# Performance work log

Hardware: AMD Instinct MI355X
Metric: run time of the kernel (lower is better)

Reference implementation:

```python
import jax, jax.numpy as jnp
import numpy as np
from jax import lax

B, T, F, H, L = 64, 2048, 128, 128, 2


def _lstm_layer(x, Wih, Whh, bih, bhh, h0, c0):
    """Single LSTM layer, torch gate order (i,f,g,o). x: [B,T,in] -> y: [B,T,H], hT, cT."""
    b = bih + bhh

    def step(carry, xt):
        h, c = carry
        gates = xt @ Wih.T + h @ Whh.T + b  # [B,4H]
        i, f, g, o = jnp.split(gates, 4, axis=-1)
        i = jax.nn.sigmoid(i)
        f = jax.nn.sigmoid(f)
        g = jnp.tanh(g)
        o = jax.nn.sigmoid(o)
        c = f * c + i * g
        h = o * jnp.tanh(c)
        return (h, c), h

    xs = jnp.swapaxes(x, 0, 1)  # [T,B,in]
    (hT, cT), ys = lax.scan(step, (h0, c0), xs)
    return jnp.swapaxes(ys, 0, 1), hT, cT


def setup_inputs() -> dict:
    key = jax.random.key(0)
    ks = jax.random.split(key, 20)
    s = 1.0 / np.sqrt(H)
    u = lambda k, shape: jax.random.uniform(k, shape, jnp.float32, -s, s)
    inp = {"x": jax.random.normal(ks[0], (B, T, F), jnp.float32)}
    i = 1
    for pre, in0 in (("enc", F), ("dec", H)):
        for l in range(L):
            d_in = in0 if l == 0 else H
            inp[f"{pre}_Wih{l}"] = u(ks[i], (4 * H, d_in)); i += 1
            inp[f"{pre}_Whh{l}"] = u(ks[i], (4 * H, H)); i += 1
            inp[f"{pre}_bih{l}"] = u(ks[i], (4 * H,)); i += 1
            inp[f"{pre}_bhh{l}"] = u(ks[i], (4 * H,)); i += 1
    inp["out_W"] = u(ks[i], (F, H)); i += 1
    inp["out_b"] = u(ks[i], (F,))
    return inp


def reference(x,
              enc_Wih0, enc_Whh0, enc_bih0, enc_bhh0,
              enc_Wih1, enc_Whh1, enc_bih1, enc_bhh1,
              dec_Wih0, dec_Whh0, dec_bih0, dec_bhh0,
              dec_Wih1, dec_Whh1, dec_bih1, dec_bhh1,
              out_W, out_b):
    z = jnp.zeros((x.shape[0], H), x.dtype)
    # encoder: 2 stacked layers, zero initial state
    y0, h0, c0 = _lstm_layer(x, enc_Wih0, enc_Whh0, enc_bih0, enc_bhh0, z, z)
    y1, h1, c1 = _lstm_layer(y0, enc_Wih1, enc_Whh1, enc_bih1, enc_bhh1, z, z)
    # decoder: zeros input, initial state = encoder final (h,c) per layer
    dec_in = jnp.zeros_like(x)  # valid since n_features == hidden_dim
    d0, _, _ = _lstm_layer(dec_in, dec_Wih0, dec_Whh0, dec_bih0, dec_bhh0, h0, c0)
    d1, _, _ = _lstm_layer(d0, dec_Wih1, dec_Whh1, dec_bih1, dec_bhh1, h1, c1)
    return d1 @ out_W.T + out_b
```

## Files before the change

kernel.cpp:

```cpp
#include <hip/hip_runtime.h>
#include <cstdint>
#include <cstddef>

typedef float    float4v __attribute__((ext_vector_type(4)));
typedef _Float16 f16x4   __attribute__((ext_vector_type(4)));
typedef _Float16 f16x8   __attribute__((ext_vector_type(8)));
typedef unsigned long long u64;
struct u64p { u64 a, b; };

#define DI __device__ __forceinline__

static const int Bsz = 64, Tlen = 2048, Hd = 128;
static const int HSTR = 144;
static const int RING = 256;
static const int YSTR = 136;

DI float sigf_fast(float x) {
    float e = __builtin_amdgcn_exp2f(-1.442695041f * x);
    return __builtin_amdgcn_rcpf(1.f + e);
}
DI float tanhf_fast(float x) {
    float e = __builtin_amdgcn_exp2f(-2.885390082f * x);
    return 2.f * __builtin_amdgcn_rcpf(1.f + e) - 1.f;
}

DI void lds_barrier() {
    asm volatile("s_waitcnt lgkmcnt(0)\n\ts_barrier" ::: "memory");
}

DI void pin(f16x8& v) {
    float4v t = __builtin_bit_cast(float4v, v);
    asm volatile("" : "+v"(t));
    v = __builtin_bit_cast(f16x8, t);
}

DI f16x8 cvt8(const float* p) {
    float4v u = *(const float4v*)p;
    float4v w = *(const float4v*)(p + 4);
    f16x8 o;
    o[0] = (_Float16)u[0]; o[1] = (_Float16)u[1]; o[2] = (_Float16)u[2]; o[3] = (_Float16)u[3];
    o[4] = (_Float16)w[0]; o[5] = (_Float16)w[1]; o[6] = (_Float16)w[2]; o[7] = (_Float16)w[3];
    return o;
}

DI u64 pack4(float4v a) {
    f16x4 h;
    h[0] = (_Float16)a[0]; h[1] = (_Float16)a[1];
    h[2] = (_Float16)a[2]; h[3] = (_Float16)a[3];
    return __builtin_bit_cast(u64, h);
}

DI u64 ald64(const void* pp) {
    return __hip_atomic_load((const u64*)pp, __ATOMIC_RELAXED, __HIP_MEMORY_SCOPE_AGENT);
}
DI void ast64(void* pp, u64 v) {
    __hip_atomic_store((u64*)pp, v, __ATOMIC_RELAXED, __HIP_MEMORY_SCOPE_AGENT);
}
DI void ast16(void* pp, unsigned short v) {
    __hip_atomic_store((unsigned short*)pp, v, __ATOMIC_RELAXED, __HIP_MEMORY_SCOPE_AGENT);
}
DI unsigned int aldu32(const unsigned int* pp) {
    return __hip_atomic_load(pp, __ATOMIC_RELAXED, __HIP_MEMORY_SCOPE_AGENT);
}
DI void astu32(unsigned int* pp, unsigned int v) {
    __hip_atomic_store(pp, v, __ATOMIC_RELAXED, __HIP_MEMORY_SCOPE_AGENT);
}

__global__ __launch_bounds__(512, 1) void lstm_mega(
    const float* __restrict__ eU0, const float* __restrict__ eb0i, const float* __restrict__ eb0h,
    const float* __restrict__ dU0, const float* __restrict__ db0i, const float* __restrict__ db0h,
    const float* __restrict__ eU1, const float* __restrict__ eb1i, const float* __restrict__ eb1h,
    const float* __restrict__ dU1, const float* __restrict__ db1i, const float* __restrict__ db1h,
    const float* __restrict__ eW1, const float* __restrict__ dW1,
    const float* __restrict__ eW0, const float* __restrict__ xin,
    const float* __restrict__ oW,  const float* __restrict__ ob,
    float* __restrict__ outp,
    _Float16* __restrict__ PB,
    _Float16* __restrict__ X2,
    _Float16* __restrict__ X1,
    _Float16* __restrict__ Y1,
    unsigned int* __restrict__ prog,  unsigned int* __restrict__ prog2,
    unsigned int* __restrict__ prog3, unsigned int* __restrict__ prog4,
    unsigned int* __restrict__ prog5, int T)
{
    const int tid  = threadIdx.x;
    const int lane = tid & 63, w = tid >> 6;
    const int col  = lane & 15, quad = lane >> 4;
    const int b    = col & 3, s = col >> 2;
    const int role = blockIdx.x >> 4;
    const int p    = blockIdx.x & 15;
    const int bglob = p * 4 + b;
    const int j    = w * 16 + s * 4 + quad;
    const int NG   = T >> 3;
    const int NG2  = NG * 2;
    const unsigned int T2 = (unsigned int)(2 * T);

    __shared__ alignas(16) _Float16 Hl[2 * 4 * HSTR];
    __shared__ alignas(16) _Float16 Ylh[32 * YSTR];

    unsigned int* pr  = prog  + p * 16;
    unsigned int* pr2 = prog2 + p * 16;
    unsigned int* pr3 = prog3 + p * 16;
    unsigned int* pr4 = prog4 + p * 16;
    unsigned int* pr5 = prog5 + p * 16;

    if (role == 0) {
        f16x8 af[4][4];
        float bq[4];
#pragma unroll
        for (int mt = 0; mt < 4; mt++) {
            int urow = (col & 3) * 128 + (w * 16 + mt * 4 + (col >> 2));
            const float* ur = eU0 + (size_t)urow * 128;
#pragma unroll
            for (int kc = 0; kc < 4; kc++) { af[mt][kc] = cvt8(ur + kc * 32 + quad * 8); pin(af[mt][kc]); }
        }
#pragma unroll
        for (int q = 0; q < 4; q++) bq[q] = eb0i[q * 128 + j] + eb0h[q * 128 + j];

        float c = 0.f, hv = 0.f;
        Hl[b * HSTR + j] = (_Float16)0.f;
        __syncthreads();

        const _Float16* x1b = X1 + (size_t)bglob * RING * 512 + 4 * j;
        unsigned short* pbp = (unsigned short*)PB + (size_t)bglob * RING * 128 + j;

        if (tid == 511) {
            unsigned int need = 16u; if (need > (unsigned int)T) need = (unsigned int)T;
            unsigned int psn = aldu32(pr3);
            while (psn < need) { __builtin_amdgcn_s_sleep(8); psn = aldu32(pr3); }
        }
        __syncthreads();
        f16x4 xp = __builtin_bit_cast(f16x4, ald64(x1b));

        int cur = 0;
        unsigned int pf3 = 0, ps3 = 0;
        for (int g = 0; g < NG2; g++) {
            if (g == NG) {
#pragma unroll
                for (int mt = 0; mt < 4; mt++) {
                    int urow = (col & 3) * 128 + (w * 16 + mt * 4 + (col >> 2));
                    const float* ur = dU0 + (size_t)urow * 128;
#pragma unroll
                    for (int kc = 0; kc < 4; kc++) { af[mt][kc] = cvt8(ur + kc * 32 + quad * 8); pin(af[mt][kc]); }
                }
#pragma unroll
                for (int q = 0; q < 4; q++) bq[q] = db0i[q * 128 + j] + db0h[q * 128 + j];
            }
            if (g < NG) {
                if (tid == 511 && g + 1 < NG) pf3 = aldu32(pr3);
#pragma unroll
                for (int k = 0; k < 8; k++) {
                    const int t = g * 8 + k;
                    f16x4 xpn = __builtin_bit_cast(f16x4,
                        ald64(x1b + (size_t)((t + 1) & (RING - 1)) * 512));

                    const _Float16* Hc = Hl + cur * (4 * HSTR);
                    f16x8 bf[4];
#pragma unroll
                    for (int kc = 0; kc < 4; kc++)
                        bf[kc] = *(const f16x8*)(Hc + b * HSTR + kc * 32 + quad * 8);

                    float4v acc[4] = {};
#pragma unroll
                    for (int kc = 0; kc < 4; kc++)
#pragma unroll
                        for (int mt = 0; mt < 4; mt++)
                            acc[mt] = __builtin_amdgcn_mfma_f32_16x16x32_f16(af[mt][kc], bf[kc], acc[mt], 0, 0, 0);

                    float4v t0 = (s & 1) ? acc[1] : acc[0];
                    float4v t1 = (s & 1) ? acc[3] : acc[2];
                    float4v gg = (s & 2) ? t1 : t0;

                    float g0 = gg[0] + bq[0] + (float)xp[0], g1 = gg[1] + bq[1] + (float)xp[1];
                    float g2 = gg[2] + bq[2] + (float)xp[2], g3 = gg[3] + bq[3] + (float)xp[3];
                    float iv = sigf_fast(g0), fv = sigf_fast(g1);
                    float gv = tanhf_fast(g2), ov = sigf_fast(g3);
                    c  = fv * c + iv * gv;
                    hv = ov * tanhf_fast(c);

                    _Float16 hf = (_Float16)hv;
                    Hl[(cur ^ 1) * (4 * HSTR) + b * HSTR + j] = hf;
                    ast16(pbp + (size_t)(t & (RING - 1)) * 128,
                          __builtin_bit_cast(unsigned short, hf));

                    if (k == 7) {
                        asm volatile("s_waitcnt vmcnt(2)" ::: "memory");
                        if (tid == 0) astu32(pr, (unsigned int)(g * 8 + 7));
                        if (tid == 511 && g + 1 < NG) {
                            unsigned int need = (unsigned int)(8 * (g + 1) + 16);
                            if (need > (unsigned int)T) need = (unsigned int)T;
                            if (ps3 < pf3) ps3 = pf3;
                            while (ps3 < need) { __builtin_amdgcn_s_sleep(2); ps3 = aldu32(pr3); }
                        }
                    }
                    lds_barrier();
                    xp = xpn;
                    cur ^= 1;
                }
            } else {
#pragma unroll
                for (int k = 0; k < 8; k++) {
                    const int t = g * 8 + k;

                    const _Float16* Hc = Hl + cur * (4 * HSTR);
                    f16x8 bf[4];
#pragma unroll
                    for (int kc = 0; kc < 4; kc++)
                        bf[kc] = *(const f16x8*)(Hc + b * HSTR + kc * 32 + quad * 8);

                    float4v acc[4] = {};
#pragma unroll
                    for (int kc = 0; kc < 4; kc++)
#pragma unroll
                        for (int mt = 0; mt < 4; mt++)
                            acc[mt] = __builtin_amdgcn_mfma_f32_16x16x32_f16(af[mt][kc], bf[kc], acc[mt], 0, 0, 0);

                    float4v t0 = (s & 1) ? acc[1] : acc[0];
                    float4v t1 = (s & 1) ? acc[3] : acc[2];
                    float4v gg = (s & 2) ? t1 : t0;

                    float g0 = gg[0] + bq[0], g1 = gg[1] + bq[1];
                    float g2 = gg[2] + bq[2], g3 = gg[3] + bq[3];
                    float iv = sigf_fast(g0), fv = sigf_fast(g1);
                    float gv = tanhf_fast(g2), ov = sigf_fast(g3);
                    c  = fv * c + iv * gv;
                    hv = ov * tanhf_fast(c);

                    _Float16 hf = (_Float16)hv;
                    Hl[(cur ^ 1) * (4 * HSTR) + b * HSTR + j] = hf;
                    ast16(pbp + (size_t)(t & (RING - 1)) * 128,
                          __builtin_bit_cast(unsigned short, hf));

                    if (k == 7) {
                        asm volatile("s_waitcnt vmcnt(1)" ::: "memory");
                        if (tid == 0) astu32(pr, (unsigned int)(g * 8 + 7));
                    }
                    lds_barrier();
                    cur ^= 1;
                }
            }
        }
        asm volatile("s_waitcnt vmcnt(0)" ::: "memory");
        __syncthreads();
        if (tid == 0) astu32(pr, T2);
    } else if (role == 1) {
        f16x8 afH[4][4];
        float bq[4];
#pragma unroll
        for (int mt = 0; mt < 4; mt++) {
            int urow = (col & 3) * 128 + (w * 16 + mt * 4 + (col >> 2));
            const float* ur = eU1 + (size_t)urow * 128;
#pragma unroll
            for (int kc = 0; kc < 4; kc++) { afH[mt][kc] = cvt8(ur + kc * 32 + quad * 8); pin(afH[mt][kc]); }
        }
#pragma unroll
        for (int q = 0; q < 4; q++) bq[q] = eb1i[q * 128 + j] + eb1h[q * 128 + j];

        float c = 0.f, hv = 0.f;
        Hl[b * HSTR + j] = (_Float16)0.f;

        if (tid == 511) {
            unsigned int need = 9u; if (need > T2) need = T2;
            unsigned int psn = aldu32(pr2);
            while (psn < need) { __builtin_amdgcn_s_sleep(8); psn = aldu32(pr2); }
        }
        __syncthreads();

        const _Float16* x2b = X2 + (size_t)bglob * RING * 512 + 4 * j;
        unsigned short* y1p = (unsigned short*)Y1 + (size_t)bglob * RING * 128 + j;
        f16x4 xp = __builtin_bit_cast(f16x4, ald64(x2b));

        int cur = 0;
        unsigned int pf2 = 0, ps2 = 0, pf5 = 0, ps5 = 0;
        for (int g = 0; g < NG2; g++) {
            if (g == NG) {
#pragma unroll
                for (int mt = 0; mt < 4; mt++) {
                    int urow = (col & 3) * 128 + (w * 16 + mt * 4 + (col >> 2));
                    const float* ur = dU1 + (size_t)urow * 128;
#pragma unroll
                    for (int kc = 0; kc < 4; kc++) { afH[mt][kc] = cvt8(ur + kc * 32 + quad * 8); pin(afH[mt][kc]); }
                }
#pragma unroll
                for (int q = 0; q < 4; q++) bq[q] = db1i[q * 128 + j] + db1h[q * 128 + j];
            }
            if (tid == 511) {
                if (g + 1 < NG2) pf2 = aldu32(pr2);
                if (g + 1 >= NG + 32 && g + 1 < NG2) pf5 = aldu32(pr5);
            }
            if (g < NG) {
#pragma unroll
                for (int k = 0; k < 8; k++) {
                    const int t = g * 8 + k;
                    f16x4 xpn = __builtin_bit_cast(f16x4,
                        ald64(x2b + (size_t)((t + 1) & (RING - 1)) * 512));

                    const _Float16* Hc = Hl + cur * (4 * HSTR);
                    f16x8 bf[4];
#pragma unroll
                    for (int kc = 0; kc < 4; kc++)
                        bf[kc] = *(const f16x8*)(Hc + b * HSTR + kc * 32 + quad * 8);

                    float4v acc[4] = {};
#pragma unroll
                    for (int kc = 0; kc < 4; kc++)
#pragma unroll
                        for (int mt = 0; mt < 4; mt++)
                            acc[mt] = __builtin_amdgcn_mfma_f32_16x16x32_f16(afH[mt][kc], bf[kc], acc[mt], 0, 0, 0);

                    float4v t0 = (s & 1) ? acc[1] : acc[0];
                    float4v t1 = (s & 1) ? acc[3] : acc[2];
                    float4v gg = (s & 2) ? t1 : t0;

                    float g0 = gg[0] + bq[0] + (float)xp[0], g1 = gg[1] + bq[1] + (float)xp[1];
                    float g2 = gg[2] + bq[2] + (float)xp[2], g3 = gg[3] + bq[3] + (float)xp[3];
                    float iv = sigf_fast(g0), fv = sigf_fast(g1);
                    float gv = tanhf_fast(g2), ov = sigf_fast(g3);
                    c  = fv * c + iv * gv;
                    hv = ov * tanhf_fast(c);

                    Hl[(cur ^ 1) * (4 * HSTR) + b * HSTR + j] = (_Float16)hv;

                    if (k == 7) {
                        if (tid == 511 && g + 1 < NG2) {
                            unsigned int need = (unsigned int)(8 * (g + 1) + 9);
                            if (need > T2) need = T2;
                            if (ps2 < pf2) ps2 = pf2;
                            while (ps2 < need) { __builtin_amdgcn_s_sleep(2); ps2 = aldu32(pr2); }
                        }
                    }
                    lds_barrier();
                    xp = xpn;
                    cur ^= 1;
                }
            } else {
#pragma unroll
                for (int k = 0; k < 8; k++) {
                    const int t = g * 8 + k;
                    f16x4 xpn = __builtin_bit_cast(f16x4,
                        ald64(x2b + (size_t)((t + 1) & (RING - 1)) * 512));

                    const _Float16* Hc = Hl + cur * (4 * HSTR);
                    f16x8 bf[4];
#pragma unroll
                    for (int kc = 0; kc < 4; kc++)
                        bf[kc] = *(const f16x8*)(Hc + b * HSTR + kc * 32 + quad * 8);

                    float4v acc[4] = {};
#pragma unroll
                    for (int kc = 0; kc < 4; kc++)
#pragma unroll
                        for (int mt = 0; mt < 4; mt++)
                            acc[mt] = __builtin_amdgcn_mfma_f32_16x16x32_f16(afH[mt][kc], bf[kc], acc[mt], 0, 0, 0);

                    float4v t0 = (s & 1) ? acc[1] : acc[0];
                    float4v t1 = (s & 1) ? acc[3] : acc[2];
                    float4v gg = (s & 2) ? t1 : t0;

                    float g0 = gg[0] + bq[0] + (float)xp[0], g1 = gg[1] + bq[1] + (float)xp[1];
                    float g2 = gg[2] + bq[2] + (float)xp[2], g3 = gg[3] + bq[3] + (float)xp[3];
                    float iv = sigf_fast(g0), fv = sigf_fast(g1);
                    float gv = tanhf_fast(g2), ov = sigf_fast(g3);
                    c  = fv * c + iv * gv;
                    hv = ov * tanhf_fast(c);

                    _Float16 hf = (_Float16)hv;
                    Hl[(cur ^ 1) * (4 * HSTR) + b * HSTR + j] = hf;
                    ast16(y1p + (size_t)(t & (RING - 1)) * 128,
                          __builtin_bit_cast(unsigned short, hf));

                    if (k == 7) {
                        asm volatile("s_waitcnt vmcnt(2)" ::: "memory");
                        if (tid == 0) astu32(pr4, (unsigned int)(g * 8 + 7));
                        if (tid == 511 && g + 1 < NG2) {
                            unsigned int need = (unsigned int)(8 * (g + 1) + 9);
                            if (need > T2) need = T2;
                            if (ps2 < pf2) ps2 = pf2;
                            while (ps2 < need) { __builtin_amdgcn_s_sleep(2); ps2 = aldu32(pr2); }
                            if (g + 1 >= NG + 32) {
                                unsigned int need5 = (unsigned int)(8 * (g + 1 - 32) + 8);
                                if (ps5 < pf5) ps5 = pf5;
                                while (ps5 < need5) { __builtin_amdgcn_s_sleep(2); ps5 = aldu32(pr5); }
                            }
                        }
                    }
                    lds_barrier();
                    xp = xpn;
                    cur ^= 1;
                }
            }
        }
        asm volatile("s_waitcnt vmcnt(0)" ::: "memory");
        __syncthreads();
        if (tid == 0) astu32(pr4, T2);
    } else if (role == 2) {
        f16x8 bw[4][4];
#pragma unroll
        for (int nt = 0; nt < 4; nt++) {
            int n = (w * 4 + nt) * 16 + col;
            int wrow = (n & 3) * 128 + (n >> 2);
            const float* Wr = eW1 + (size_t)wrow * 128;
#pragma unroll
            for (int kc = 0; kc < 4; kc++) { bw[nt][kc] = cvt8(Wr + kc * 32 + quad * 8); pin(bw[nt][kc]); }
        }

        const int lrow = tid >> 4, lchunk = tid & 15;
        const int lb = lrow & 3, ltr = lrow >> 2;

        for (int g = 0; g < NG2; g++) {
            if (g == NG) {
#pragma unroll
                for (int nt = 0; nt < 4; nt++) {
                    int n = (w * 4 + nt) * 16 + col;
                    int wrow = (n & 3) * 128 + (n >> 2);
                    const float* Wr = dW1 + (size_t)wrow * 128;
#pragma unroll
                    for (int kc = 0; kc < 4; kc++) { bw[nt][kc] = cvt8(Wr + kc * 32 + quad * 8); pin(bw[nt][kc]); }
                }
            }
            if (tid == 0) {
                unsigned int need = (unsigned int)(g * 8 + 8);
                unsigned int psn = aldu32(pr);
                while (psn < need) { __builtin_amdgcn_s_sleep(4); psn = aldu32(pr); }
            }
            __syncthreads();
            {
                int slot = (g * 8 + ltr) & (RING - 1);
                const char* srcp = (const char*)(PB + ((size_t)(p * 4 + lb) * RING + slot) * 128 + lchunk * 8);
                u64 a0 = ald64(srcp);
                u64 a1 = ald64(srcp + 8);
                char* dst = (char*)&Ylh[lrow * YSTR + lchunk * 8];
                *(u64*)dst = a0;
                *(u64*)(dst + 8) = a1;
            }
            lds_barrier();

            float4v acc[2][4] = {};
#pragma unroll
            for (int kc = 0; kc < 4; kc++) {
                f16x8 y0 = *(const f16x8*)&Ylh[col * YSTR + kc * 32 + quad * 8];
                f16x8 y1t = *(const f16x8*)&Ylh[(16 + col) * YSTR + kc * 32 + quad * 8];
#pragma unroll
                for (int nt = 0; nt < 4; nt++) {
                    acc[0][nt] = __builtin_amdgcn_mfma_f32_16x16x32_f16(bw[nt][kc], y0,  acc[0][nt], 0, 0, 0);
                    acc[1][nt] = __builtin_amdgcn_mfma_f32_16x16x32_f16(bw[nt][kc], y1t, acc[1][nt], 0, 0, 0);
                }
            }
            {
                const int bb = col & 3;
#pragma unroll
                for (int mt = 0; mt < 2; mt++) {
                    int trow = mt * 4 + (col >> 2);
                    int slot = (g * 8 + trow) & (RING - 1);
                    _Float16* dst = X2 + ((size_t)(p * 4 + bb) * RING + slot) * 512 + (w * 4) * 16 + quad * 4;
#pragma unroll
                    for (int nt = 0; nt < 4; nt++)
                        ast64(dst + nt * 16, pack4(acc[mt][nt]));
                }
            }
            asm volatile("s_waitcnt vmcnt(0)" ::: "memory");
            __syncthreads();
            if (tid == 0) astu32(pr2, (unsigned int)(g * 8 + 8));
        }
    } else if (role == 3) {
        f16x8 bw[4][4];
#pragma unroll
        for (int nt = 0; nt < 4; nt++) {
            int n = (w * 4 + nt) * 16 + col;
            int wrow = (n & 3) * 128 + (n >> 2);
            const float* Wr = eW0 + (size_t)wrow * 128;
#pragma unroll
            for (int kc = 0; kc < 4; kc++) { bw[nt][kc] = cvt8(Wr + kc * 32 + quad * 8); pin(bw[nt][kc]); }
        }

        const int lrow = tid >> 4, lchunk = tid & 15;
        const int lb = lrow & 3, ltr = lrow >> 2;
        const float* xsrc = xin + (size_t)(p * 4 + lb) * T * 128 + lchunk * 8;

        for (int g = 0; g < NG; g++) {
            if (g >= 32 && tid == 0) {
                unsigned int need = (unsigned int)(8 * (g - 32));
                unsigned int psn = aldu32(pr);
                while (psn < need) { __builtin_amdgcn_s_sleep(4); psn = aldu32(pr); }
            }
            __syncthreads();
            {
                f16x8 xv = cvt8(xsrc + (size_t)(g * 8 + ltr) * 128);
                u64p w2 = __builtin_bit_cast(u64p, xv);
                char* dst = (char*)&Ylh[lrow * YSTR + lchunk * 8];
                *(u64*)dst = w2.a;
                *(u64*)(dst + 8) = w2.b;
            }
            lds_barrier();

            float4v acc[2][4] = {};
#pragma unroll
            for (int kc = 0; kc < 4; kc++) {
                f16x8 y0 = *(const f16x8*)&Ylh[col * YSTR + kc * 32 + quad * 8];
                f16x8 y1t = *(const f16x8*)&Ylh[(16 + col) * YSTR + kc * 32 + quad * 8];
#pragma unroll
                for (int nt = 0; nt < 4; nt++) {
                    acc[0][nt] = __builtin_amdgcn_mfma_f32_16x16x32_f16(bw[nt][kc], y0,  acc[0][nt], 0, 0, 0);
                    acc[1][nt] = __builtin_amdgcn_mfma_f32_16x16x32_f16(bw[nt][kc], y1t, acc[1][nt], 0, 0, 0);
                }
            }
            {
                const int bb = col & 3;
#pragma unroll
                for (int mt = 0; mt < 2; mt++) {
                    int trow = mt * 4 + (col >> 2);
                    int slot = (g * 8 + trow) & (RING - 1);
                    _Float16* dst = X1 + ((size_t)(p * 4 + bb) * RING + slot) * 512 + (w * 4) * 16 + quad * 4;
#pragma unroll
                    for (int nt = 0; nt < 4; nt++)
                        ast64(dst + nt * 16, pack4(acc[mt][nt]));
                }
            }
            asm volatile("s_waitcnt vmcnt(0)" ::: "memory");
            __syncthreads();
            if (tid == 0) astu32(pr3, (unsigned int)(g * 8 + 8));
        }
    } else {
        f16x8 bo[4];
#pragma unroll
        for (int kc = 0; kc < 4; kc++) { bo[kc] = cvt8(oW + (size_t)(w * 16 + col) * 128 + kc * 32 + quad * 8); pin(bo[kc]); }
        float4v bv4 = *(const float4v*)(ob + w * 16 + quad * 4);

        const int lrow = tid >> 4, lchunk = tid & 15;
        const int lb = lrow & 3, ltr = lrow >> 2;

        for (int gg = 0; gg < NG; gg++) {
            const int g = NG + gg;
            if (tid == 0) {
                unsigned int need = (unsigned int)(g * 8 + 8);
                unsigned int psn = aldu32(pr4);
                while (psn < need) { __builtin_amdgcn_s_sleep(4); psn = aldu32(pr4); }
            }
            __syncthreads();
            {
                int slot = (g * 8 + ltr) & (RING - 1);
                const char* srcp = (const char*)(Y1 + ((size_t)(p * 4 + lb) * RING + slot) * 128 + lchunk * 8);
                u64 a0 = ald64(srcp);
                u64 a1 = ald64(srcp + 8);
                char* dst = (char*)&Ylh[lrow * YSTR + lchunk * 8];
                *(u64*)dst = a0;
                *(u64*)(dst + 8) = a1;
            }
            lds_barrier();
            if (tid == 0) astu32(pr5, (unsigned int)(g * 8 + 8));

            float4v acc[2] = {};
#pragma unroll
            for (int kc = 0; kc < 4; kc++) {
                f16x8 y0 = *(const f16x8*)&Ylh[col * YSTR + kc * 32 + quad * 8];
                f16x8 y1t = *(const f16x8*)&Ylh[(16 + col) * YSTR + kc * 32 + quad * 8];
                acc[0] = __builtin_amdgcn_mfma_f32_16x16x32_f16(bo[kc], y0,  acc[0], 0, 0, 0);
                acc[1] = __builtin_amdgcn_mfma_f32_16x16x32_f16(bo[kc], y1t, acc[1], 0, 0, 0);
            }
            {
                const int bb = col & 3;
#pragma unroll
                for (int mt = 0; mt < 2; mt++) {
                    int trow = mt * 4 + (col >> 2);
                    float4v v = acc[mt];
                    v[0] += bv4[0]; v[1] += bv4[1]; v[2] += bv4[2]; v[3] += bv4[3];
                    *(float4v*)(outp + ((size_t)(p * 4 + bb) * T + gg * 8 + trow) * 128 + w * 16 + quad * 4) = v;
                }
            }
        }
    }
}

extern "C" void kernel_launch(void* const* d_in, const int* in_sizes, int n_in,
                              void* d_out, int out_size, void* d_ws, size_t ws_size,
                              hipStream_t stream)
{
    const float* x    = (const float*)d_in[0];
    const float* eW0  = (const float*)d_in[1];
    const float* eU0  = (const float*)d_in[2];
    const float* eb0i = (const float*)d_in[3];
    const float* eb0h = (const float*)d_in[4];
    const float* eW1  = (const float*)d_in[5];
    const float* eU1  = (const float*)d_in[6];
    const float* eb1i = (const float*)d_in[7];
    const float* eb1h = (const float*)d_in[8];
    const float* dU0  = (const float*)d_in[10];
    const float* db0i = (const float*)d_in[11];
    const float* db0h = (const float*)d_in[12];
    const float* dW1  = (const float*)d_in[13];
    const float* dU1  = (const float*)d_in[14];
    const float* db1i = (const float*)d_in[15];
    const float* db1h = (const float*)d_in[16];
    const float* oW   = (const float*)d_in[17];
    const float* ob   = (const float*)d_in[18];

    char* ws = (char*)d_ws;
    _Float16* X1 = (_Float16*)(ws);
    _Float16* X2 = (_Float16*)(ws + (16u << 20));
    _Float16* PB = (_Float16*)(ws + (32u << 20));
    _Float16* Y1 = (_Float16*)(ws + (36u << 20));
    unsigned int* pg = (unsigned int*)(ws + (40u << 20));

    hipMemsetAsync((void*)pg, 0, 8192, stream);

    lstm_mega<<<dim3(80), dim3(512), 0, stream>>>(
        eU0, eb0i, eb0h, dU0, db0i, db0h,
        eU1, eb1i, eb1h, dU1, db1i, db1h,
        eW1, dW1, eW0, x, oW, ob, (float*)d_out,
        PB, X2, X1, Y1,
        pg, pg + 256, pg + 512, pg + 768, pg + 1024, Tlen);
}
```

Before: 2.400 ms.

## Halve block size to 256 threads, each thread computing two hidden units

```diff
diff --git a/kernel.cpp b/kernel.cpp
--- a/kernel.cpp
+++ b/kernel.cpp
@@ -66,7 +66,7 @@
     __hip_atomic_store(pp, v, __ATOMIC_RELAXED, __HIP_MEMORY_SCOPE_AGENT);
 }
 
-__global__ __launch_bounds__(512, 1) void lstm_mega(
+__global__ __launch_bounds__(256, 1) void lstm_mega(
     const float* __restrict__ eU0, const float* __restrict__ eb0i, const float* __restrict__ eb0h,
     const float* __restrict__ dU0, const float* __restrict__ db0i, const float* __restrict__ db0h,
     const float* __restrict__ eU1, const float* __restrict__ eb1i, const float* __restrict__ eb1h,
@@ -90,7 +90,8 @@
     const int role = blockIdx.x >> 4;
     const int p    = blockIdx.x & 15;
     const int bglob = p * 4 + b;
-    const int j    = w * 16 + s * 4 + quad;
+    const int jA   = w * 32 + s * 4 + quad;
+    const int jB   = jA + 16;
     const int NG   = T >> 3;
     const int NG2  = NG * 2;
     const unsigned int T2 = (unsigned int)(2 * T);
@@ -105,54 +106,65 @@
     unsigned int* pr5 = prog5 + p * 16;
 
     if (role == 0) {
-        f16x8 af[4][4];
-        float bq[4];
-#pragma unroll
-        for (int mt = 0; mt < 4; mt++) {
-            int urow = (col & 3) * 128 + (w * 16 + mt * 4 + (col >> 2));
+        f16x8 af[8][4];
+        float bqA[4], bqB[4];
+#pragma unroll
+        for (int mt = 0; mt < 8; mt++) {
+            int urow = (col & 3) * 128 + (w * 32 + mt * 4 + (col >> 2));
             const float* ur = eU0 + (size_t)urow * 128;
 #pragma unroll
             for (int kc = 0; kc < 4; kc++) { af[mt][kc] = cvt8(ur + kc * 32 + quad * 8); pin(af[mt][kc]); }
         }
 #pragma unroll
-        for (int q = 0; q < 4; q++) bq[q] = eb0i[q * 128 + j] + eb0h[q * 128 + j];
-
-        float c = 0.f, hv = 0.f;
-        Hl[b * HSTR + j] = (_Float16)0.f;
+        for (int q = 0; q < 4; q++) {
+            bqA[q] = eb0i[q * 128 + jA] + eb0h[q * 128 + jA];
+            bqB[q] = eb0i[q * 128 + jB] + eb0h[q * 128 + jB];
+        }
+
+        float cA = 0.f, hA = 0.f, cB = 0.f, hB = 0.f;
+        Hl[b * HSTR + jA] = (_Float16)0.f;
+        Hl[b * HSTR + jB] = (_Float16)0.f;
         __syncthreads();
 
-        const _Float16* x1b = X1 + (size_t)bglob * RING * 512 + 4 * j;
-        unsigned short* pbp = (unsigned short*)PB + (size_t)bglob * RING * 128 + j;
-
-        if (tid == 511) {
+        const _Float16* x1bA = X1 + (size_t)bglob * RING * 512 + 4 * jA;
+        const _Float16* x1bB = x1bA + 64;
+        unsigned short* pbpA = (unsigned short*)PB + (size_t)bglob * RING * 128 + jA;
+        unsigned short* pbpB = pbpA + 16;
+
+        if (tid == 255) {
             unsigned int need = 16u; if (need > (unsigned int)T) need = (unsigned int)T;
             unsigned int psn = aldu32(pr3);
             while (psn < need) { __builtin_amdgcn_s_sleep(8); psn = aldu32(pr3); }
         }
         __syncthreads();
-        f16x4 xp = __builtin_bit_cast(f16x4, ald64(x1b));
+        f16x4 xpA = __builtin_bit_cast(f16x4, ald64(x1bA));
+        f16x4 xpB = __builtin_bit_cast(f16x4, ald64(x1bB));
 
         int cur = 0;
         unsigned int pf3 = 0, ps3 = 0;
         for (int g = 0; g < NG2; g++) {
             if (g == NG) {
 #pragma unroll
-                for (int mt = 0; mt < 4; mt++) {
-                    int urow = (col & 3) * 128 + (w * 16 + mt * 4 + (col >> 2));
+                for (int mt = 0; mt < 8; mt++) {
+                    int urow = (col & 3) * 128 + (w * 32 + mt * 4 + (col >> 2));
                     const float* ur = dU0 + (size_t)urow * 128;
 #pragma unroll
                     for (int kc = 0; kc < 4; kc++) { af[mt][kc] = cvt8(ur + kc * 32 + quad * 8); pin(af[mt][kc]); }
                 }
 #pragma unroll
-                for (int q = 0; q < 4; q++) bq[q] = db0i[q * 128 + j] + db0h[q * 128 + j];
+                for (int q = 0; q < 4; q++) {
+                    bqA[q] = db0i[q * 128 + jA] + db0h[q * 128 + jA];
+                    bqB[q] = db0i[q * 128 + jB] + db0h[q * 128 + jB];
+                }
             }
             if (g < NG) {
-                if (tid == 511 && g + 1 < NG) pf3 = aldu32(pr3);
+                if (tid == 255 && g + 1 < NG) pf3 = aldu32(pr3);
 #pragma unroll
                 for (int k = 0; k < 8; k++) {
                     const int t = g * 8 + k;
-                    f16x4 xpn = __builtin_bit_cast(f16x4,
-                        ald64(x1b + (size_t)((t + 1) & (RING - 1)) * 512));
+                    const size_t nsl = (size_t)((t + 1) & (RING - 1)) * 512;
+                    f16x4 xpnA = __builtin_bit_cast(f16x4, ald64(x1bA + nsl));
+                    f16x4 xpnB = __builtin_bit_cast(f16x4, ald64(x1bB + nsl));
 
                     const _Float16* Hc = Hl + cur * (4 * HSTR);
                     f16x8 bf[4];
@@ -160,33 +172,46 @@
                     for (int kc = 0; kc < 4; kc++)
                         bf[kc] = *(const f16x8*)(Hc + b * HSTR + kc * 32 + quad * 8);
 
-                    float4v acc[4] = {};
+                    float4v acc[8] = {};
 #pragma unroll
                     for (int kc = 0; kc < 4; kc++)
 #pragma unroll
-                        for (int mt = 0; mt < 4; mt++)
+                        for (int mt = 0; mt < 8; mt++)
                             acc[mt] = __builtin_amdgcn_mfma_f32_16x16x32_f16(af[mt][kc], bf[kc], acc[mt], 0, 0, 0);
 
-                    float4v t0 = (s & 1) ? acc[1] : acc[0];
-                    float4v t1 = (s & 1) ? acc[3] : acc[2];
-                    float4v gg = (s & 2) ? t1 : t0;
-
-                    float g0 = gg[0] + bq[0] + (float)xp[0], g1 = gg[1] + bq[1] + (float)xp[1];
-                    float g2 = gg[2] + bq[2] + (float)xp[2], g3 = gg[3] + bq[3] + (float)xp[3];
-                    float iv = sigf_fast(g0), fv = sigf_fast(g1);
-                    float gv = tanhf_fast(g2), ov = sigf_fast(g3);
-                    c  = fv * c + iv * gv;
-                    hv = ov * tanhf_fast(c);
-
-                    _Float16 hf = (_Float16)hv;
-                    Hl[(cur ^ 1) * (4 * HSTR) + b * HSTR + j] = hf;
-                    ast16(pbp + (size_t)(t & (RING - 1)) * 128,
-                          __builtin_bit_cast(unsigned short, hf));
+                    float4v u0 = (s & 1) ? acc[1] : acc[0];
+                    float4v u1 = (s & 1) ? acc[3] : acc[2];
+                    float4v gA = (s & 2) ? u1 : u0;
+                    float4v u2 = (s & 1) ? acc[5] : acc[4];
+                    float4v u3 = (s & 1) ? acc[7] : acc[6];
+                    float4v gB = (s & 2) ? u3 : u2;
+
+                    float a0 = gA[0] + bqA[0] + (float)xpA[0], a1 = gA[1] + bqA[1] + (float)xpA[1];
+                    float a2 = gA[2] + bqA[2] + (float)xpA[2], a3 = gA[3] + bqA[3] + (float)xpA[3];
+                    float iA = sigf_fast(a0), fA = sigf_fast(a1);
+                    float gvA = tanhf_fast(a2), oA = sigf_fast(a3);
+                    cA = fA * cA + iA * gvA;
+                    hA = oA * tanhf_fast(cA);
+
+                    float b0 = gB[0] + bqB[0] + (float)xpB[0], b1 = gB[1] + bqB[1] + (float)xpB[1];
+                    float b2 = gB[2] + bqB[2] + (float)xpB[2], b3 = gB[3] + bqB[3] + (float)xpB[3];
+                    float iB = sigf_fast(b0), fB = sigf_fast(b1);
+                    float gvB = tanhf_fast(b2), oB = sigf_fast(b3);
+                    cB = fB * cB + iB * gvB;
+                    hB = oB * tanhf_fast(cB);
+
+                    _Float16 hfA = (_Float16)hA, hfB = (_Float16)hB;
+                    _Float16* Hn = Hl + (cur ^ 1) * (4 * HSTR) + b * HSTR;
+                    Hn[jA] = hfA;
+                    Hn[jB] = hfB;
+                    const size_t sl = (size_t)(t & (RING - 1)) * 128;
+                    ast16(pbpA + sl, __builtin_bit_cast(unsigned short, hfA));
+                    ast16(pbpB + sl, __builtin_bit_cast(unsigned short, hfB));
 
                     if (k == 7) {
-                        asm volatile("s_waitcnt vmcnt(2)" ::: "memory");
+                        asm volatile("s_waitcnt vmcnt(4)" ::: "memory");
                         if (tid == 0) astu32(pr, (unsigned int)(g * 8 + 7));
-                        if (tid == 511 && g + 1 < NG) {
+                        if (tid == 255 && g + 1 < NG) {
                             unsigned int need = (unsigned int)(8 * (g + 1) + 16);
                             if (need > (unsigned int)T) need = (unsigned int)T;
                             if (ps3 < pf3) ps3 = pf3;
@@ -194,7 +219,7 @@
                         }
                     }
                     lds_barrier();
-                    xp = xpn;
+                    xpA = xpnA; xpB = xpnB;
                     cur ^= 1;
                 }
             } else {
@@ -208,31 +233,44 @@
                     for (int kc = 0; kc < 4; kc++)
                         bf[kc] = *(const f16x8*)(Hc + b * HSTR + kc * 32 + quad * 8);
 
-                    float4v acc[4] = {};
+                    float4v acc[8] = {};
 #pragma unroll
                     for (int kc = 0; kc < 4; kc++)
 #pragma unroll
-                        for (int mt = 0; mt < 4; mt++)
+                        for (int mt = 0; mt < 8; mt++)
                             acc[mt] = __builtin_amdgcn_mfma_f32_16x16x32_f16(af[mt][kc], bf[kc], acc[mt], 0, 0, 0);
 
-                    float4v t0 = (s & 1) ? acc[1] : acc[0];
-                    float4v t1 = (s & 1) ? acc[3] : acc[2];
-                    float4v gg = (s & 2) ? t1 : t0;
-
-                    float g0 = gg[0] + bq[0], g1 = gg[1] + bq[1];
-                    float g2 = gg[2] + bq[2], g3 = gg[3] + bq[3];
-                    float iv = sigf_fast(g0), fv = sigf_fast(g1);
-                    float gv = tanhf_fast(g2), ov = sigf_fast(g3);
-                    c  = fv * c + iv * gv;
-                    hv = ov * tanhf_fast(c);
-
-                    _Float16 hf = (_Float16)hv;
-                    Hl[(cur ^ 1) * (4 * HSTR) + b * HSTR + j] = hf;
-                    ast16(pbp + (size_t)(t & (RING - 1)) * 128,
-                          __builtin_bit_cast(unsigned short, hf));
+                    float4v u0 = (s & 1) ? acc[1] : acc[0];
+                    float4v u1 = (s & 1) ? acc[3] : acc[2];
+                    float4v gA = (s & 2) ? u1 : u0;
+                    float4v u2 = (s & 1) ? acc[5] : acc[4];
+                    float4v u3 = (s & 1) ? acc[7] : acc[6];
+                    float4v gB = (s & 2) ? u3 : u2;
+
+                    float a0 = gA[0] + bqA[0], a1 = gA[1] + bqA[1];
+                    float a2 = gA[2] + bqA[2], a3 = gA[3] + bqA[3];
+                    float iA = sigf_fast(a0), fA = sigf_fast(a1);
+                    float gvA = tanhf_fast(a2), oA = sigf_fast(a3);
+                    cA = fA * cA + iA * gvA;
+                    hA = oA * tanhf_fast(cA);
+
+                    float b0 = gB[0] + bqB[0], b1 = gB[1] + bqB[1];
+                    float b2 = gB[2] + bqB[2], b3 = gB[3] + bqB[3];
+                    float iB = sigf_fast(b0), fB = sigf_fast(b1);
+                    float gvB = tanhf_fast(b2), oB = sigf_fast(b3);
+                    cB = fB * cB + iB * gvB;
+                    hB = oB * tanhf_fast(cB);
+
+                    _Float16 hfA = (_Float16)hA, hfB = (_Float16)hB;
+                    _Float16* Hn = Hl + (cur ^ 1) * (4 * HSTR) + b * HSTR;
+                    Hn[jA] = hfA;
+                    Hn[jB] = hfB;
+                    const size_t sl = (size_t)(t & (RING - 1)) * 128;
+                    ast16(pbpA + sl, __builtin_bit_cast(unsigned short, hfA));
+                    ast16(pbpB + sl, __builtin_bit_cast(unsigned short, hfB));
 
                     if (k == 7) {
-                        asm volatile("s_waitcnt vmcnt(1)" ::: "memory");
+                        asm volatile("s_waitcnt vmcnt(2)" ::: "memory");
                         if (tid == 0) astu32(pr, (unsigned int)(g * 8 + 7));
                     }
                     lds_barrier();
@@ -244,174 +282,155 @@
         __syncthreads();
         if (tid == 0) astu32(pr, T2);
     } else if (role == 1) {
-        f16x8 afH[4][4];
-        float bq[4];
-#pragma unroll
-        for (int mt = 0; mt < 4; mt++) {
-            int urow = (col & 3) * 128 + (w * 16 + mt * 4 + (col >> 2));
+        f16x8 afH[8][4];
+        float bqA[4], bqB[4];
+#pragma unroll
+        for (int mt = 0; mt < 8; mt++) {
+            int urow = (col & 3) * 128 + (w * 32 + mt * 4 + (col >> 2));
             const float* ur = eU1 + (size_t)urow * 128;
 #pragma unroll
             for (int kc = 0; kc < 4; kc++) { afH[mt][kc] = cvt8(ur + kc * 32 + quad * 8); pin(afH[mt][kc]); }
         }
 #pragma unroll
-        for (int q = 0; q < 4; q++) bq[q] = eb1i[q * 128 + j] + eb1h[q * 128 + j];
-
-        float c = 0.f, hv = 0.f;
-        Hl[b * HSTR + j] = (_Float16)0.f;
-
-        if (tid == 511) {
+        for (int q = 0; q < 4; q++) {
+            bqA[q] = eb1i[q * 128 + jA] + eb1h[q * 128 + jA];
+            bqB[q] = eb1i[q * 128 + jB] + eb1h[q * 128 + jB];
+        }
+
+        float cA = 0.f, hA = 0.f, cB = 0.f, hB = 0.f;
+        Hl[b * HSTR + jA] = (_Float16)0.f;
+        Hl[b * HSTR + jB] = (_Float16)0.f;
+
+        if (tid == 255) {
             unsigned int need = 9u; if (need > T2) need = T2;
             unsigned int psn = aldu32(pr2);
             while (psn < need) { __builtin_amdgcn_s_sleep(8); psn = aldu32(pr2); }
         }
         __syncthreads();
 
-        const _Float16* x2b = X2 + (size_t)bglob * RING * 512 + 4 * j;
-        unsigned short* y1p = (unsigned short*)Y1 + (size_t)bglob * RING * 128 + j;
-        f16x4 xp = __builtin_bit_cast(f16x4, ald64(x2b));
+        const _Float16* x2bA = X2 + (size_t)bglob * RING * 512 + 4 * jA;
+        const _Float16* x2bB = x2bA + 64;
+        unsigned short* y1pA = (unsigned short*)Y1 + (size_t)bglob * RING * 128 + jA;
+        unsigned short* y1pB = y1pA + 16;
+        f16x4 xpA = __builtin_bit_cast(f16x4, ald64(x2bA));
+        f16x4 xpB = __builtin_bit_cast(f16x4, ald64(x2bB));
 
         int cur = 0;
         unsigned int pf2 = 0, ps2 = 0, pf5 = 0, ps5 = 0;
         for (int g = 0; g < NG2; g++) {
             if (g == NG) {
 #pragma unroll
-                for (int mt = 0; mt < 4; mt++) {
-                    int urow = (col & 3) * 128 + (w * 16 + mt * 4 + (col >> 2));
+                for (int mt = 0; mt < 8; mt++) {
+                    int urow = (col & 3) * 128 + (w * 32 + mt * 4 + (col >> 2));
                     const float* ur = dU1 + (size_t)urow * 128;
 #pragma unroll
                     for (int kc = 0; kc < 4; kc++) { afH[mt][kc] = cvt8(ur + kc * 32 + quad * 8); pin(afH[mt][kc]); }
                 }
 #pragma unroll
-                for (int q = 0; q < 4; q++) bq[q] = db1i[q * 128 + j] + db1h[q * 128 + j];
-            }
-            if (tid == 511) {
+                for (int q = 0; q < 4; q++) {
+                    bqA[q] = db1i[q * 128 + jA] + db1h[q * 128 + jA];
+                    bqB[q] = db1i[q * 128 + jB] + db1h[q * 128 + jB];
+                }
+            }
+            if (tid == 255) {
                 if (g + 1 < NG2) pf2 = aldu32(pr2);
                 if (g + 1 >= NG + 32 && g + 1 < NG2) pf5 = aldu32(pr5);
             }
-            if (g < NG) {
-#pragma unroll
-                for (int k = 0; k < 8; k++) {
-                    const int t = g * 8 + k;
-                    f16x4 xpn = __builtin_bit_cast(f16x4,
-                        ald64(x2b + (size_t)((t + 1) & (RING - 1)) * 512));
-
-                    const _Float16* Hc = Hl + cur * (4 * HSTR);
-                    f16x8 bf[4];
-#pragma unroll
-                    for (int kc = 0; kc < 4; kc++)
-                        bf[kc] = *(const f16x8*)(Hc + b * HSTR + kc * 32 + quad * 8);
-
-                    float4v acc[4] = {};
-#pragma unroll
-                    for (int kc = 0; kc < 4; kc++)
-#pragma unroll
-                        for (int mt = 0; mt < 4; mt++)
-                            acc[mt] = __builtin_amdgcn_mfma_f32_16x16x32_f16(afH[mt][kc], bf[kc], acc[mt], 0, 0, 0);
-
-                    float4v t0 = (s & 1) ? acc[1] : acc[0];
-                    float4v t1 = (s & 1) ? acc[3] : acc[2];
-                    float4v gg = (s & 2) ? t1 : t0;
-
-                    float g0 = gg[0] + bq[0] + (float)xp[0], g1 = gg[1] + bq[1] + (float)xp[1];
-                    float g2 = gg[2] + bq[2] + (float)xp[2], g3 = gg[3] + bq[3] + (float)xp[3];
-                    float iv = sigf_fast(g0), fv = sigf_fast(g1);
-                    float gv = tanhf_fast(g2), ov = sigf_fast(g3);
-                    c  = fv * c + iv * gv;
-                    hv = ov * tanhf_fast(c);
-
-                    Hl[(cur ^ 1) * (4 * HSTR) + b * HSTR + j] = (_Float16)hv;
-
-                    if (k == 7) {
-                        if (tid == 511 && g + 1 < NG2) {
-                            unsigned int need = (unsigned int)(8 * (g + 1) + 9);
-                            if (need > T2) need = T2;
-                            if (ps2 < pf2) ps2 = pf2;
-                            while (ps2 < need) { __builtin_amdgcn_s_sleep(2); ps2 = aldu32(pr2); }
+            const bool isDec = (g >= NG);
+#pragma unroll
+            for (int k = 0; k < 8; k++) {
+                const int t = g * 8 + k;
+                const size_t nsl = (size_t)((t + 1) & (RING - 1)) * 512;
+                f16x4 xpnA = __builtin_bit_cast(f16x4, ald64(x2bA + nsl));
+                f16x4 xpnB = __builtin_bit_cast(f16x4, ald64(x2bB + nsl));
+
+                const _Float16* Hc = Hl + cur * (4 * HSTR);
+                f16x8 bf[4];
+#pragma unroll
+                for (int kc = 0; kc < 4; kc++)
+                    bf[kc] = *(const f16x8*)(Hc + b * HSTR + kc * 32 + quad * 8);
+
+                float4v acc[8] = {};
+#pragma unroll
+                for (int kc = 0; kc < 4; kc++)
+#pragma unroll
+                    for (int mt = 0; mt < 8; mt++)
+                        acc[mt] = __builtin_amdgcn_mfma_f32_16x16x32_f16(afH[mt][kc], bf[kc], acc[mt], 0, 0, 0);
+
+                float4v u0 = (s & 1) ? acc[1] : acc[0];
+                float4v u1 = (s & 1) ? acc[3] : acc[2];
+                float4v gA = (s & 2) ? u1 : u0;
+                float4v u2 = (s & 1) ? acc[5] : acc[4];
+                float4v u3 = (s & 1) ? acc[7] : acc[6];
+                float4v gB = (s & 2) ? u3 : u2;
+
+                float a0 = gA[0] + bqA[0] + (float)xpA[0], a1 = gA[1] + bqA[1] + (float)xpA[1];
+                float a2 = gA[2] + bqA[2] + (float)xpA[2], a3 = gA[3] + bqA[3] + (float)xpA[3];
+                float iA = sigf_fast(a0), fA = sigf_fast(a1);
+                float gvA = tanhf_fast(a2), oA = sigf_fast(a3);
+                cA = fA * cA + iA * gvA;
+                hA = oA * tanhf_fast(cA);
+
+                float b0 = gB[0] + bqB[0] + (float)xpB[0], b1 = gB[1] + bqB[1] + (float)xpB[1];
+                float b2 = gB[2] + bqB[2] + (float)xpB[2], b3 = gB[3] + bqB[3] + (float)xpB[3];
+                float iB = sigf_fast(b0), fB = sigf_fast(b1);
+                float gvB = tanhf_fast(b2), oB = sigf_fast(b3);
+                cB = fB * cB + iB * gvB;
+                hB = oB * tanhf_fast(cB);
+
+                _Float16 hfA = (_Float16)hA, hfB = (_Float16)hB;
+                _Float16* Hn = Hl + (cur ^ 1) * (4 * HSTR) + b * HSTR;
+                Hn[jA] = hfA;
+                Hn[jB] = hfB;
+                if (isDec) {
+                    const size_t sl = (size_t)(t & (RING - 1)) * 128;
+                    ast16(y1pA + sl, __builtin_bit_cast(unsigned short, hfA));
+                    ast16(y1pB + sl, __builtin_bit_cast(unsigned short, hfB));
+                }
+
+                if (k == 7) {
+                    if (isDec) {
+                        asm volatile("s_waitcnt vmcnt(4)" ::: "memory");
+                        if (tid == 0) astu32(pr4, (unsigned int)(g * 8 + 7));
+                    }
+                    if (tid == 255 && g + 1 < NG2) {
+                        unsigned int need = (unsigned int)(8 * (g + 1) + 9);
+                        if (need > T2) need = T2;
+                        if (ps2 < pf2) ps2 = pf2;
+                        while (ps2 < need) { __builtin_amdgcn_s_sleep(2); ps2 = aldu32(pr2); }
+                        if (isDec && g + 1 >= NG + 32) {
+                            unsigned int need5 = (unsigned int)(8 * (g + 1 - 32) + 8);
+                            if (ps5 < pf5) ps5 = pf5;
+                            while (ps5 < need5) { __builtin_amdgcn_s_sleep(2); ps5 = aldu32(pr5); }
                         }
                     }
-                    lds_barrier();
-                    xp = xpn;
-                    cur ^= 1;
-                }
-            } else {
-#pragma unroll
-                for (int k = 0; k < 8; k++) {
-                    const int t = g * 8 + k;
-                    f16x4 xpn = __builtin_bit_cast(f16x4,
-                        ald64(x2b + (size_t)((t + 1) & (RING - 1)) * 512));
-
-                    const _Float16* Hc = Hl + cur * (4 * HSTR);
-                    f16x8 bf[4];
-#pragma unroll
-                    for (int kc = 0; kc < 4; kc++)
-                        bf[kc] = *(const f16x8*)(Hc + b * HSTR + kc * 32 + quad * 8);
-
-                    float4v acc[4] = {};
-#pragma unroll
-                    for (int kc = 0; kc < 4; kc++)
-#pragma unroll
-                        for (int mt = 0; mt < 4; mt++)
-                            acc[mt] = __builtin_amdgcn_mfma_f32_16x16x32_f16(afH[mt][kc], bf[kc], acc[mt], 0, 0, 0);
-
-                    float4v t0 = (s & 1) ? acc[1] : acc[0];
-                    float4v t1 = (s & 1) ? acc[3] : acc[2];
-                    float4v gg = (s & 2) ? t1 : t0;
-
-                    float g0 = gg[0] + bq[0] + (float)xp[0], g1 = gg[1] + bq[1] + (float)xp[1];
-                    float g2 = gg[2] + bq[2] + (float)xp[2], g3 = gg[3] + bq[3] + (float)xp[3];
-                    float iv = sigf_fast(g0), fv = sigf_fast(g1);
-                    float gv = tanhf_fast(g2), ov = sigf_fast(g3);
-                    c  = fv * c + iv * gv;
-                    hv = ov * tanhf_fast(c);
-
-                    _Float16 hf = (_Float16)hv;
-                    Hl[(cur ^ 1) * (4 * HSTR) + b * HSTR + j] = hf;
-                    ast16(y1p + (size_t)(t & (RING - 1)) * 128,
-                          __builtin_bit_cast(unsigned short, hf));
-
-                    if (k == 7) {
-                        asm volatile("s_waitcnt vmcnt(2)" ::: "memory");
-                        if (tid == 0) astu32(pr4, (unsigned int)(g * 8 + 7));
-                        if (tid == 511 && g + 1 < NG2) {
-                            unsigned int need = (unsigned int)(8 * (g + 1) + 9);
-                            if (need > T2) need = T2;
-                            if (ps2 < pf2) ps2 = pf2;
-                            while (ps2 < need) { __builtin_amdgcn_s_sleep(2); ps2 = aldu32(pr2); }
-                            if (g + 1 >= NG + 32) {
-                                unsigned int need5 = (unsigned int)(8 * (g + 1 - 32) + 8);
-                                if (ps5 < pf5) ps5 = pf5;
-                                while (ps5 < need5) { __builtin_amdgcn_s_sleep(2); ps5 = aldu32(pr5); }
-                            }
-                        }
-                    }
-                    lds_barrier();
-                    xp = xpn;
-                    cur ^= 1;
-                }
+                }
+                lds_barrier();
+                xpA = xpnA; xpB = xpnB;
+                cur ^= 1;
             }
         }
         asm volatile("s_waitcnt vmcnt(0)" ::: "memory");
         __syncthreads();
         if (tid == 0) astu32(pr4, T2);
     } else if (role == 2) {
-        f16x8 bw[4][4];
-#pragma unroll
-        for (int nt = 0; nt < 4; nt++) {
-            int n = (w * 4 + nt) * 16 + col;
+        f16x8 bw[8][4];
+#pragma unroll
+        for (int nt = 0; nt < 8; nt++) {
+            int n = (w * 8 + nt) * 16 + col;
             int wrow = (n & 3) * 128 + (n >> 2);
             const float* Wr = eW1 + (size_t)wrow * 128;
 #pragma unroll
             for (int kc = 0; kc < 4; kc++) { bw[nt][kc] = cvt8(Wr + kc * 32 + quad * 8); pin(bw[nt][kc]); }
         }
 
-        const int lrow = tid >> 4, lchunk = tid & 15;
-        const int lb = lrow & 3, ltr = lrow >> 2;
+        const int lrow0 = tid >> 4, lchunk = tid & 15;
 
         for (int g = 0; g < NG2; g++) {
             if (g == NG) {
 #pragma unroll
-                for (int nt = 0; nt < 4; nt++) {
-                    int n = (w * 4 + nt) * 16 + col;
+                for (int nt = 0; nt < 8; nt++) {
+                    int n = (w * 8 + nt) * 16 + col;
                     int wrow = (n & 3) * 128 + (n >> 2);
                     const float* Wr = dW1 + (size_t)wrow * 128;
 #pragma unroll
@@ -424,24 +443,27 @@
                 while (psn < need) { __builtin_amdgcn_s_sleep(4); psn = aldu32(pr); }
             }
             __syncthreads();
-            {
+#pragma unroll
+            for (int rr = 0; rr < 2; rr++) {
+                int row = lrow0 + rr * 16;
+                int lb = row & 3, ltr = row >> 2;
                 int slot = (g * 8 + ltr) & (RING - 1);
                 const char* srcp = (const char*)(PB + ((size_t)(p * 4 + lb) * RING + slot) * 128 + lchunk * 8);
                 u64 a0 = ald64(srcp);
                 u64 a1 = ald64(srcp + 8);
-                char* dst = (char*)&Ylh[lrow * YSTR + lchunk * 8];
+                char* dst = (char*)&Ylh[row * YSTR + lchunk * 8];
                 *(u64*)dst = a0;
                 *(u64*)(dst + 8) = a1;
             }
             lds_barrier();
 
-            float4v acc[2][4] = {};
+            float4v acc[2][8] = {};
 #pragma unroll
             for (int kc = 0; kc < 4; kc++) {
-                f16x8 y0 = *(const f16x8*)&Ylh[col * YSTR + kc * 32 + quad * 8];
+                f16x8 y0  = *(const f16x8*)&Ylh[col * YSTR + kc * 32 + quad * 8];
                 f16x8 y1t = *(const f16x8*)&Ylh[(16 + col) * YSTR + kc * 32 + quad * 8];
 #pragma unroll
-                for (int nt = 0; nt < 4; nt++) {
+                for (int nt = 0; nt < 8; nt++) {
                     acc[0][nt] = __builtin_amdgcn_mfma_f32_16x16x32_f16(bw[nt][kc], y0,  acc[0][nt], 0, 0, 0);
                     acc[1][nt] = __builtin_amdgcn_mfma_f32_16x16x32_f16(bw[nt][kc], y1t, acc[1][nt], 0, 0, 0);
                 }
@@ -452,9 +474,9 @@
                 for (int mt = 0; mt < 2; mt++) {
                     int trow = mt * 4 + (col >> 2);
                     int slot = (g * 8 + trow) & (RING - 1);
-                    _Float16* dst = X2 + ((size_t)(p * 4 + bb) * RING + slot) * 512 + (w * 4) * 16 + quad * 4;
-#pragma unroll
-                    for (int nt = 0; nt < 4; nt++)
+                    _Float16* dst = X2 + ((size_t)(p * 4 + bb) * RING + slot) * 512 + (w * 8) * 16 + quad * 4;
+#pragma unroll
+                    for (int nt = 0; nt < 8; nt++)
                         ast64(dst + nt * 16, pack4(acc[mt][nt]));
                 }
             }
@@ -463,19 +485,17 @@
             if (tid == 0) astu32(pr2, (unsigned int)(g * 8 + 8));
         }
     } else if (role == 3) {
-        f16x8 bw[4][4];
-#pragma unroll
-        for (int nt = 0; nt < 4; nt++) {
-            int n = (w * 4 + nt) * 16 + col;
+        f16x8 bw[8][4];
+#pragma unroll
+        for (int nt = 0; nt < 8; nt++) {
+            int n = (w * 8 + nt) * 16 + col;
             int wrow = (n & 3) * 128 + (n >> 2);
             const float* Wr = eW0 + (size_t)wrow * 128;
 #pragma unroll
             for (int kc = 0; kc < 4; kc++) { bw[nt][kc] = cvt8(Wr + kc * 32 + quad * 8); pin(bw[nt][kc]); }
         }
 
-        const int lrow = tid >> 4, lchunk = tid & 15;
-        const int lb = lrow & 3, ltr = lrow >> 2;
-        const float* xsrc = xin + (size_t)(p * 4 + lb) * T * 128 + lchunk * 8;
+        const int lrow0 = tid >> 4, lchunk = tid & 15;
 
         for (int g = 0; g < NG; g++) {
             if (g >= 32 && tid == 0) {
@@ -484,22 +504,25 @@
                 while (psn < need) { __builtin_amdgcn_s_sleep(4); psn = aldu32(pr); }
             }
             __syncthreads();
-            {
-                f16x8 xv = cvt8(xsrc + (size_t)(g * 8 + ltr) * 128);
+#pragma unroll
+            for (int rr = 0; rr < 2; rr++) {
+                int row = lrow0 + rr * 16;
+                int lb = row & 3, ltr = row >> 2;
+                f16x8 xv = cvt8(xin + ((size_t)(p * 4 + lb) * T + g * 8 + ltr) * 128 + lchunk * 8);
                 u64p w2 = __builtin_bit_cast(u64p, xv);
-                char* dst = (char*)&Ylh[lrow * YSTR + lchunk * 8];
+                char* dst = (char*)&Ylh[row * YSTR + lchunk * 8];
                 *(u64*)dst = w2.a;
                 *(u64*)(dst + 8) = w2.b;
             }
             lds_barrier();
 
-            float4v acc[2][4] = {};
+            float4v acc[2][8] = {};
 #pragma unroll
             for (int kc = 0; kc < 4; kc++) {
-                f16x8 y0 = *(const f16x8*)&Ylh[col * YSTR + kc * 32 + quad * 8];
+                f16x8 y0  = *(const f16x8*)&Ylh[col * YSTR + kc * 32 + quad * 8];
                 f16x8 y1t = *(const f16x8*)&Ylh[(16 + col) * YSTR + kc * 32 + quad * 8];
 #pragma unroll
-                for (int nt = 0; nt < 4; nt++) {
+                for (int nt = 0; nt < 8; nt++) {
                     acc[0][nt] = __builtin_amdgcn_mfma_f32_16x16x32_f16(bw[nt][kc], y0,  acc[0][nt], 0, 0, 0);
                     acc[1][nt] = __builtin_amdgcn_mfma_f32_16x16x32_f16(bw[nt][kc], y1t, acc[1][nt], 0, 0, 0);
                 }
@@ -510,9 +533,9 @@
                 for (int mt = 0; mt < 2; mt++) {
                     int trow = mt * 4 + (col >> 2);
                     int slot = (g * 8 + trow) & (RING - 1);
-                    _Float16* dst = X1 + ((size_t)(p * 4 + bb) * RING + slot) * 512 + (w * 4) * 16 + quad * 4;
-#pragma unroll
-                    for (int nt = 0; nt < 4; nt++)
+                    _Float16* dst = X1 + ((size_t)(p * 4 + bb) * RING + slot) * 512 + (w * 8) * 16 + quad * 4;
+#pragma unroll
+                    for (int nt = 0; nt < 8; nt++)
                         ast64(dst + nt * 16, pack4(acc[mt][nt]));
                 }
             }
@@ -521,13 +544,17 @@
             if (tid == 0) astu32(pr3, (unsigned int)(g * 8 + 8));
         }
     } else {
-        f16x8 bo[4];
-#pragma unroll
-        for (int kc = 0; kc < 4; kc++) { bo[kc] = cvt8(oW + (size_t)(w * 16 + col) * 128 + kc * 32 + quad * 8); pin(bo[kc]); }
-        float4v bv4 = *(const float4v*)(ob + w * 16 + quad * 4);
-
-        const int lrow = tid >> 4, lchunk = tid & 15;
-        const int lb = lrow & 3, ltr = lrow >> 2;
+        f16x8 bo[2][4];
+        float4v bv4[2];
+#pragma unroll
+        for (int nt = 0; nt < 2; nt++) {
+            const float* Wr = oW + (size_t)(w * 32 + nt * 16 + col) * 128;
+#pragma unroll
+            for (int kc = 0; kc < 4; kc++) { bo[nt][kc] = cvt8(Wr + kc * 32 + quad * 8); pin(bo[nt][kc]); }
+            bv4[nt] = *(const float4v*)(ob + w * 32 + nt * 16 + quad * 4);
+        }
+
+        const int lrow0 = tid >> 4, lchunk = tid & 15;
 
         for (int gg = 0; gg < NG; gg++) {
             const int g = NG + gg;
@@ -537,34 +564,45 @@
                 while (psn < need) { __builtin_amdgcn_s_sleep(4); psn = aldu32(pr4); }
             }
             __syncthreads();
-            {
+#pragma unroll
+            for (int rr = 0; rr < 2; rr++) {
+                int row = lrow0 + rr * 16;
+                int lb = row & 3, ltr = row >> 2;
                 int slot = (g * 8 + ltr) & (RING - 1);
                 const char* srcp = (const char*)(Y1 + ((size_t)(p * 4 + lb) * RING + slot) * 128 + lchunk * 8);
                 u64 a0 = ald64(srcp);
                 u64 a1 = ald64(srcp + 8);
-                char* dst = (char*)&Ylh[lrow * YSTR + lchunk * 8];
+                char* dst = (char*)&Ylh[row * YSTR + lchunk * 8];
                 *(u64*)dst = a0;
                 *(u64*)(dst + 8) = a1;
             }
             lds_barrier();
             if (tid == 0) astu32(pr5, (unsigned int)(g * 8 + 8));
 
-            float4v acc[2] = {};
+            float4v acc[2][2] = {};
 #pragma unroll
             for (int kc = 0; kc < 4; kc++) {
-                f16x8 y0 = *(const f16x8*)&Ylh[col * YSTR + kc * 32 + quad * 8];
+                f16x8 y0  = *(const f16x8*)&Ylh[col * YSTR + kc * 32 + quad * 8];
                 f16x8 y1t = *(const f16x8*)&Ylh[(16 + col) * YSTR + kc * 32 + quad * 8];
-                acc[0] = __builtin_amdgcn_mfma_f32_16x16x32_f16(bo[kc], y0,  acc[0], 0, 0, 0);
-                acc[1] = __builtin_amdgcn_mfma_f32_16x16x32_f16(bo[kc], y1t, acc[1], 0, 0, 0);
+#pragma unroll
+                for (int nt = 0; nt < 2; nt++) {
+                    acc[0][nt] = __builtin_amdgcn_mfma_f32_16x16x32_f16(bo[nt][kc], y0,  acc[0][nt], 0, 0, 0);
+                    acc[1][nt] = __builtin_amdgcn_mfma_f32_16x16x32_f16(bo[nt][kc], y1t, acc[1][nt], 0, 0, 0);
+                }
             }
             {
                 const int bb = col & 3;
 #pragma unroll
                 for (int mt = 0; mt < 2; mt++) {
                     int trow = mt * 4 + (col >> 2);
-                    float4v v = acc[mt];
-                    v[0] += bv4[0]; v[1] += bv4[1]; v[2] += bv4[2]; v[3] += bv4[3];
-                    *(float4v*)(outp + ((size_t)(p * 4 + bb) * T + gg * 8 + trow) * 128 + w * 16 + quad * 4) = v;
+#pragma unroll
+                    for (int nt = 0; nt < 2; nt++) {
+                        float4v v = acc[mt][nt];
+                        v[0] += bv4[nt][0]; v[1] += bv4[nt][1];
+                        v[2] += bv4[nt][2]; v[3] += bv4[nt][3];
+                        *(float4v*)(outp + ((size_t)(p * 4 + bb) * T + gg * 8 + trow) * 128
+                                    + w * 32 + nt * 16 + quad * 4) = v;
+                    }
                 }
             }
         }
@@ -603,7 +641,7 @@
 
     hipMemsetAsync((void*)pg, 0, 8192, stream);
 
-    lstm_mega<<<dim3(80), dim3(512), 0, stream>>>(
+    lstm_mega<<<dim3(80), dim3(256), 0, stream>>>(
         eU0, eb0i, eb0h, dU0, db0i, db0h,
         eU1, eb1i, eb1h, dU1, db1i, db1h,
         eW1, dW1, eW0, x, oW, ob, (float*)d_out,
```

Result: slower. 2.614 ms (+8.9%).
